# Performance work log

Hardware: AMD Instinct MI355X
Metric: run time of the kernel (lower is better)

Reference implementation:

```python
import jax, jax.numpy as jnp
import numpy as np

NEG = -1e9  # stand-in for -inf mask fill (avoids NaN, softmax weight ~0)
EPS = 1e-5  # torch LayerNorm default


def layer_norm(x, g, b):
    mu = jnp.mean(x, axis=-1, keepdims=True)
    var = jnp.mean(jnp.square(x - mu), axis=-1, keepdims=True)
    return (x - mu) * jax.lax.rsqrt(var + EPS) * g + b


def _forward(x, context, batch_lengths, max_len,
             Wq1, Wk1, Wv1, Wq2, Wk2, Wv2,
             ln1_g, ln1_b, ln2_g, ln2_b, ln3_g, ln3_b,
             fc1_w, fc1_b, fc2_w, fc2_b):
    B, L, E = x.shape
    H, _, dk = Wq1.shape
    pos = jnp.arange(L)
    valid = pos[None, :] < batch_lengths[:, None]                  # [B,L]
    out_mask = valid[:, :, None].astype(x.dtype)                   # [B,L,1] (outputMask)
    key_bias = jnp.where(valid, 0.0, NEG)[:, None, None, :]        # [B,1,1,L] (attnMask on keys)
    causal_bias = jnp.where(pos[:, None] >= pos[None, :], 0.0, NEG)  # [L,L] decoding mask
    scale = 1.0 / jnp.sqrt(jnp.asarray(dk, x.dtype))

    def mha(qk_src, v_src, Wq, Wk, Wv, causal):
        # Q,K from qk_src, V from v_src (faithful to Head.forward)
        m = out_mask[:, None]                                      # [B,1,L,1]
        Q = jnp.einsum('ble,hed->bhld', qk_src, Wq) * m
        K = jnp.einsum('ble,hed->bhld', qk_src, Wk) * m
        V = jnp.einsum('ble,hed->bhld', v_src, Wv) * m
        e = jnp.einsum('bhid,bhjd->bhij', Q, K) + key_bias
        if causal:
            e = e + causal_bias
        s = jax.nn.softmax(e * scale, axis=-1)
        o = jnp.einsum('bhij,bhjd->bhid', s, V)
        return o.transpose(0, 2, 1, 3).reshape(B, L, E)            # concat heads

    z = mha(x, x, Wq1, Wk1, Wv1, causal=True) * out_mask
    x1 = layer_norm(x + z, ln1_g, ln1_b)
    # cross block: Q,K from context, V from x1 (as in source)
    z = mha(context, x1, Wq2, Wk2, Wv2, causal=False) * out_mask
    x2 = layer_norm(x1 + z, ln2_g, ln2_b)
    h = jax.nn.relu(x2 @ fc1_w + fc1_b) * out_mask
    z = (h @ fc2_w + fc2_b) * out_mask
    return layer_norm(x2 + z, ln3_g, ln3_b)


def setup_inputs() -> dict:
    B, L, E, H = 8, 1024, 1024, 16
    dk = E // H
    key = jax.random.key(0)
    ks = jax.random.split(key, 16)
    w = lambda k, s: jax.random.normal(k, s, jnp.float32) * 0.02
    return {
        'x': jax.random.normal(ks[0], (B, L, E), jnp.float32),
        'context': jax.random.normal(ks[1], (B, L, E), jnp.float32),
        'batch_lengths': jax.random.randint(ks[2], (B,), 1, L + 1),
        'max_len': L,
        'Wq1': w(ks[3], (H, E, dk)), 'Wk1': w(ks[4], (H, E, dk)), 'Wv1': w(ks[5], (H, E, dk)),
        'Wq2': w(ks[6], (H, E, dk)), 'Wk2': w(ks[7], (H, E, dk)), 'Wv2': w(ks[8], (H, E, dk)),
        'ln1_g': jnp.ones((E,), jnp.float32), 'ln1_b': jnp.zeros((E,), jnp.float32),
        'ln2_g': jnp.ones((E,), jnp.float32), 'ln2_b': jnp.zeros((E,), jnp.float32),
        'ln3_g': jnp.ones((E,), jnp.float32), 'ln3_b': jnp.zeros((E,), jnp.float32),
        'fc1_w': w(ks[9], (E, E)), 'fc1_b': jnp.zeros((E,), jnp.float32),
        'fc2_w': w(ks[10], (E, E)), 'fc2_b': jnp.zeros((E,), jnp.float32),
    }


def reference(x, context, batch_lengths, max_len,
              Wq1, Wk1, Wv1, Wq2, Wk2, Wv2,
              ln1_g, ln1_b, ln2_g, ln2_b, ln3_g, ln3_b,
              fc1_w, fc1_b, fc2_w, fc2_b):
    return _forward(x, context, batch_lengths, max_len,
                    Wq1, Wk1, Wv1, Wq2, Wk2, Wv2,
                    ln1_g, ln1_b, ln2_g, ln2_b, ln3_g, ln3_b,
                    fc1_w, fc1_b, fc2_w, fc2_b)
```

## Files before the change

kernel.cpp:

```cpp
#include <hip/hip_runtime.h>


typedef unsigned short u16;
typedef unsigned int u32;
typedef __attribute__((ext_vector_type(8))) short bf16x8;
typedef __attribute__((ext_vector_type(4))) float f32x4;

#define Bv 8
#define Lv 1024
#define Ev 1024
#define Hv 16
#define DKv 64
#define Mv (Bv * Lv)

#if defined(__has_builtin)
# if __has_builtin(__builtin_amdgcn_global_load_lds)
#  define HAS_GLL 1
# endif
#endif
#ifndef HAS_GLL
# define HAS_GLL 0
#endif

#if HAS_GLL
__device__ __forceinline__ void gll16(const u16* g, u16* l) {
    __builtin_amdgcn_global_load_lds(
        (const __attribute__((address_space(1))) void*)(unsigned long long)(g),
        (__attribute__((address_space(3))) void*)(unsigned)(unsigned long long)(l),
        16, 0, 0);
}
#endif

#define FENCE() asm volatile("" ::: "memory")

__device__ __forceinline__ u16 f2bf(float f) {
    u32 u = __float_as_uint(f);
    u += 0x7fffu + ((u >> 16) & 1u);
    return (u16)(u >> 16);
}
__device__ __forceinline__ u32 pack2(float a, float b) {
    u32 ua = __float_as_uint(a); ua += 0x7fffu + ((ua >> 16) & 1u);
    u32 ub = __float_as_uint(b); ub += 0x7fffu + ((ub >> 16) & 1u);
    return (ua >> 16) | (ub & 0xffff0000u);
}
__device__ __forceinline__ float bf_lo(u32 u) { return __uint_as_float(u << 16); }
__device__ __forceinline__ float bf_hi(u32 u) { return __uint_as_float(u & 0xffff0000u); }

__global__ __launch_bounds__(256) void prep_k(
    const float* __restrict__ x, const float* __restrict__ ctx,
    const float* __restrict__ wq1, const float* __restrict__ wk1, const float* __restrict__ wv1,
    const float* __restrict__ wq2, const float* __restrict__ wk2, const float* __restrict__ wv2,
    const float* __restrict__ f1, const float* __restrict__ f2,
    u16* __restrict__ xb, u16* __restrict__ cb, u16* __restrict__ WT) {
    const int id = blockIdx.x, t = threadIdx.x;
    if (id < 16384) {
        const float* s = (id < 8192) ? x : ctx;
        u16* d = (id < 8192) ? xb : cb;
        const int i4 = ((id & 8191) * 256 + t) * 4;
        float4 v = *(const float4*)(s + i4);
        uint2 o = {pack2(v.x, v.y), pack2(v.z, v.w)};
        *(uint2*)(d + i4) = o;
        return;
    }
    __shared__ float tl[32][33];
    const int tx = t & 31, ty = t >> 5;
    if (id < 16384 + 6144) {
        const int wi = (id - 16384) >> 10;
        const int tile = (id - 16384) & 1023;
        const float* s = (wi == 0) ? wq1 : (wi == 1) ? wk1 : (wi == 2) ? wv1
                       : (wi == 3) ? wq2 : (wi == 4) ? wk2 : wv2;
        u16* d = WT + (size_t)wi * Ev * Ev;
        const int h = tile >> 6, rem = tile & 63;
        const int d0 = (rem & 1) * 32, e0 = (rem >> 1) * 32;
#pragma unroll
        for (int i = 0; i < 4; i++)
            tl[ty + i * 8][tx] = s[(size_t)h * Ev * DKv + (size_t)(e0 + ty + i * 8) * DKv + d0 + tx];
        __syncthreads();
#pragma unroll
        for (int i = 0; i < 4; i++)
            d[(size_t)(h * DKv + d0 + ty + i * 8) * Ev + e0 + tx] = f2bf(tl[tx][ty + i * 8]);
    } else {
        const int wi = (id - 16384 - 6144) >> 10;
        const int tile = (id - 16384 - 6144) & 1023;
        const float* s = wi ? f2 : f1;
        u16* d = WT + (size_t)(6 + wi) * Ev * Ev;
        const int n0 = (tile & 31) * 32, k0 = (tile >> 5) * 32;
#pragma unroll
        for (int i = 0; i < 4; i++)
            tl[ty + i * 8][tx] = s[(size_t)(k0 + ty + i * 8) * Ev + n0 + tx];
        __syncthreads();
#pragma unroll
        for (int i = 0; i < 4; i++)
            d[(size_t)(n0 + ty + i * 8) * Ev + k0 + tx] = f2bf(tl[tx][ty + i * 8]);
    }
}

template <int BIAS, int RELU, int TRANSW>
__global__ __launch_bounds__(256, 4) void mgemm(const u16* __restrict__ A,
                                                const u16* __restrict__ Wt,
                                                const float* __restrict__ bias,
                                                u16* __restrict__ O0, u16* __restrict__ O1,
                                                u16* __restrict__ O2,
                                                const int* __restrict__ lens,
                                                const u16* __restrict__ A2) {
    __shared__ u16 Alds[2][8 * 512];
    __shared__ u16 Blds[2][8 * 512];
    const int tid = threadIdx.x;
    const int w = tid >> 6, l = tid & 63;
    const int lc = l & 15, lq = l >> 4;
    const int row0 = blockIdx.y * 128, col0 = blockIdx.x * 128;
    const int which = col0 >> 10, colL = col0 & 1023;
    u16* C = (which == 0) ? O0 : (which == 1 ? O1 : O2);
    const bool tr = (TRANSW == which);
    const u16* Aop = (A2 != nullptr && which == 2) ? A2 : A;

    int len = lens[row0 >> 10];
    len = min(max(len, 0), Lv);
    if ((row0 & (Lv - 1)) >= len) {
        const int rr = tid >> 1, cc = (tid & 1) * 64;
        u16* p = tr ? C + (size_t)(colL + rr) * Mv + row0 + cc
                    : C + (size_t)(row0 + rr) * Ev + colL + cc;
        uint4 z4 = {0u, 0u, 0u, 0u};
#pragma unroll
        for (int i = 0; i < 8; i++) *(uint4*)(p + i * 8) = z4;
        return;
    }

    const int wm4 = (w >> 1) * 4, wn4 = (w & 1) * 4;
    f32x4 acc[4][4];
#pragma unroll
    for (int i = 0; i < 4; i++)
#pragma unroll
        for (int j = 0; j < 4; j++) acc[i][j] = (f32x4){0.f, 0.f, 0.f, 0.f};

    const u16* Ag[2]; const u16* Bg[2];
    int lof[2];
#pragma unroll
    for (int i = 0; i < 2; i++) {
        const int s = 2 * w + i;
        Ag[i] = Aop + (size_t)(row0 + s * 16 + lc) * Ev + lq * 8;
        Bg[i] = Wt  + (size_t)(col0 + s * 16 + lc) * Ev + lq * 8;
        lof[i] = s * 512;
    }

#if HAS_GLL
#pragma unroll
    for (int i = 0; i < 2; i++) { gll16(Ag[i], &Alds[0][lof[i]]); gll16(Bg[i], &Blds[0][lof[i]]); }
#pragma unroll
    for (int i = 0; i < 2; i++) { gll16(Ag[i] + 32, &Alds[1][lof[i]]); gll16(Bg[i] + 32, &Blds[1][lof[i]]); }

    for (int t = 0; t < 32; ++t) {
        const int p = t & 1;
        if (t < 31) asm volatile("s_waitcnt vmcnt(4)" ::: "memory");
        else        asm volatile("s_waitcnt vmcnt(0)" ::: "memory");
        __builtin_amdgcn_s_barrier();
        FENCE();
        bf16x8 af[4], bfr[4];
#pragma unroll
        for (int mt = 0; mt < 4; mt++)
            af[mt] = *(const bf16x8*)(&Alds[p][(wm4 + mt) * 512 + l * 8]);
#pragma unroll
        for (int nt = 0; nt < 4; nt++)
            bfr[nt] = *(const bf16x8*)(&Blds[p][(wn4 + nt) * 512 + l * 8]);
#pragma unroll
        for (int mt = 0; mt < 4; mt++)
#pragma unroll
            for (int nt = 0; nt < 4; nt++)
                acc[mt][nt] = __builtin_amdgcn_mfma_f32_16x16x32_bf16(
                    af[mt], bfr[nt], acc[mt][nt], 0, 0, 0);
        FENCE();
        __builtin_amdgcn_s_barrier();
        FENCE();
        if (t < 30) {
            const int ko = (t + 2) * 32;
#pragma unroll
            for (int i = 0; i < 2; i++) {
                gll16(Ag[i] + ko, &Alds[p][lof[i]]);
                gll16(Bg[i] + ko, &Blds[p][lof[i]]);
            }
        }
    }
#else
    for (int t = 0; t < 32; ++t) {
        const int ko = t * 32;
#pragma unroll
        for (int i = 0; i < 2; i++) {
            *(uint4*)(&Alds[0][lof[i] + l * 8]) = *(const uint4*)(Ag[i] + ko);
            *(uint4*)(&Blds[0][lof[i] + l * 8]) = *(const uint4*)(Bg[i] + ko);
        }
        __syncthreads();
        bf16x8 af[4], bfr[4];
#pragma unroll
        for (int mt = 0; mt < 4; mt++)
            af[mt] = *(const bf16x8*)(&Alds[0][(wm4 + mt) * 512 + l * 8]);
#pragma unroll
        for (int nt = 0; nt < 4; nt++)
            bfr[nt] = *(const bf16x8*)(&Blds[0][(wn4 + nt) * 512 + l * 8]);
#pragma unroll
        for (int mt = 0; mt < 4; mt++)
#pragma unroll
            for (int nt = 0; nt < 4; nt++)
                acc[mt][nt] = __builtin_amdgcn_mfma_f32_16x16x32_bf16(
                    af[mt], bfr[nt], acc[mt][nt], 0, 0, 0);
        __syncthreads();
    }
#endif

    float bv[4];
#pragma unroll
    for (int nt = 0; nt < 4; nt++)
        bv[nt] = BIAS ? bias[colL + wn4 * 16 + nt * 16 + lc] : 0.f;

#pragma unroll
    for (int mt = 0; mt < 4; mt++) {
        const int rowb = row0 + wm4 * 16 + mt * 16 + lq * 4;
#pragma unroll
        for (int nt = 0; nt < 4; nt++) {
            const int col = colL + wn4 * 16 + nt * 16 + lc;
            float v[4];
#pragma unroll
            for (int r = 0; r < 4; r++) {
                float xv = acc[mt][nt][r] + bv[nt];
                if (RELU) xv = fmaxf(xv, 0.f);
                v[r] = (((rowb + r) & (Lv - 1)) >= len) ? 0.f : xv;
            }
            if (tr) {
                uint2 o = {pack2(v[0], v[1]), pack2(v[2], v[3])};
                *(uint2*)(C + (size_t)col * Mv + rowb) = o;
            } else {
#pragma unroll
                for (int r = 0; r < 4; r++)
                    C[(size_t)(rowb + r) * Ev + col] = f2bf(v[r]);
            }
        }
    }
}

template <int CAUSAL>
__global__ __launch_bounds__(256) void mattn(u16* __restrict__ QZ,
                                             const u16* __restrict__ K,
                                             const u16* __restrict__ VT,
                                             const int* __restrict__ lens) {
    __shared__ u16 Kt[2][16 * 512];
    __shared__ u16 Vt[2][16 * 512];
    __shared__ u16 Pt[4 * 4 * 512];
    const int b = blockIdx.z, h = blockIdx.y, qb = blockIdx.x;
    const int q0 = qb * 128;
    const int tid = threadIdx.x;
    const int w = tid >> 6, l = tid & 63;
    const int lc = l & 15, lq = l >> 4;
    int len = lens[b];
    len = min(max(len, 0), Lv);

    if (q0 >= len) {
        const int zr = tid >> 1, zc = (tid & 1) * 32;
        uint4 z4 = {0u, 0u, 0u, 0u};
        uint4* p = (uint4*)(QZ + (size_t)(b * Lv + q0 + zr) * Ev + h * DKv + zc);
        p[0] = z4; p[1] = z4; p[2] = z4; p[3] = z4;
        return;
    }

    bf16x8 qf[2][2];
#pragma unroll
    for (int mt = 0; mt < 2; mt++)
#pragma unroll
        for (int k2 = 0; k2 < 2; k2++)
            qf[mt][k2] = *(const bf16x8*)(QZ + (size_t)(b * Lv + q0 + w * 32 + mt * 16 + lc) * Ev +
                                          h * DKv + k2 * 32 + lq * 8);

    f32x4 of[2][4];
#pragma unroll
    for (int mt = 0; mt < 2; mt++)
#pragma unroll
        for (int nd = 0; nd < 4; nd++) of[mt][nd] = (f32x4){0.f, 0.f, 0.f, 0.f};
    float mrow[2][4], lrow[2][4];
#pragma unroll
    for (int mt = 0; mt < 2; mt++)
#pragma unroll
        for (int r = 0; r < 4; r++) { mrow[mt][r] = -1e30f; lrow[mt][r] = 0.f; }

    const u16* Kg[4]; const u16* Vg[4];
    int kof[4], vof[4];
#pragma unroll
    for (int i = 0; i < 4; i++) {
        const int k16 = 2 * w + (i >> 1), d32 = i & 1;
        Kg[i] = K + (size_t)(b * Lv + k16 * 16 + lc) * Ev + h * DKv + d32 * 32 + lq * 8;
        kof[i] = (k16 * 2 + d32) * 512;
        Vg[i] = VT + (size_t)(h * DKv + w * 16 + lc) * Mv + b * Lv + i * 32 + lq * 8;
        vof[i] = (w * 4 + i) * 512;
    }
    u16* Pw = Pt + w * 2048;

    const int jend = CAUSAL ? min(len, q0 + 128) : len;
    const int ntiles = (jend + 127) >> 7;

#if HAS_GLL
#pragma unroll
    for (int i = 0; i < 4; i++) {
        gll16(Kg[i], &Kt[0][kof[i]]);
        gll16(Vg[i], &Vt[0][vof[i]]);
    }
#endif
#if !HAS_GLL
#pragma unroll
    for (int i = 0; i < 4; i++) {
        *(uint4*)(&Kt[0][kof[i] + l * 8]) = *(const uint4*)Kg[i];
        *(uint4*)(&Vt[0][vof[i] + l * 8]) = *(const uint4*)Vg[i];
    }
    __syncthreads();
#endif

    for (int kt = 0; kt < ntiles; kt++) {
        const int p = kt & 1;
        const int koff = kt * 128;
#if HAS_GLL
        if (kt + 1 < ntiles) {
            const int knext = koff + 128;
#pragma unroll
            for (int i = 0; i < 4; i++) {
                gll16(Kg[i] + (size_t)knext * Ev, &Kt[p ^ 1][kof[i]]);
                gll16(Vg[i] + knext, &Vt[p ^ 1][vof[i]]);
            }
            asm volatile("s_waitcnt vmcnt(8)" ::: "memory");
        } else {
            asm volatile("s_waitcnt vmcnt(0)" ::: "memory");
        }
        __builtin_amdgcn_s_barrier();
        FENCE();
#else
        if (kt > 0) {
            const int kprev = koff;
#pragma unroll
            for (int i = 0; i < 4; i++) {
                *(uint4*)(&Kt[p][kof[i] + l * 8]) = *(const uint4*)(Kg[i] + (size_t)kprev * Ev);
                *(uint4*)(&Vt[p][vof[i] + l * 8]) = *(const uint4*)(Vg[i] + kprev);
            }
            __syncthreads();
        }
#endif
        const u16* Kb = &Kt[p][0];
        const u16* Vb = &Vt[p][0];

        f32x4 sf[2][8];
#pragma unroll
        for (int nt = 0; nt < 8; nt++) {
            bf16x8 kf0 = *(const bf16x8*)(Kb + (nt * 2 + 0) * 512 + l * 8);
            bf16x8 kf1 = *(const bf16x8*)(Kb + (nt * 2 + 1) * 512 + l * 8);
#pragma unroll
            for (int mt = 0; mt < 2; mt++) {
                f32x4 s = (f32x4){0.f, 0.f, 0.f, 0.f};
                s = __builtin_amdgcn_mfma_f32_16x16x32_bf16(qf[mt][0], kf0, s, 0, 0, 0);
                s = __builtin_amdgcn_mfma_f32_16x16x32_bf16(qf[mt][1], kf1, s, 0, 0, 0);
                sf[mt][nt] = s;
            }
        }

        float alpha[2][4];
#pragma unroll
        for (int mt = 0; mt < 2; mt++) {
            float tmax[4] = {-1e30f, -1e30f, -1e30f, -1e30f};
#pragma unroll
            for (int nt = 0; nt < 8; nt++) {
                const int jj = koff + nt * 16 + lc;
                const bool jv = jj < len;
#pragma unroll
                for (int r = 0; r < 4; r++) {
                    const int iq = q0 + w * 32 + mt * 16 + lq * 4 + r;
                    const bool valid = jv && (!CAUSAL || jj <= iq);
                    float e = valid ? sf[mt][nt][r] * 0.125f : -1e30f;
                    sf[mt][nt][r] = e;
                    tmax[r] = fmaxf(tmax[r], e);
                }
            }
#pragma unroll
            for (int r = 0; r < 4; r++) {
#pragma unroll
                for (int d = 1; d < 16; d <<= 1)
                    tmax[r] = fmaxf(tmax[r], __shfl_xor(tmax[r], d, 64));
            }
            float psum[4];
#pragma unroll
            for (int r = 0; r < 4; r++) {
                const float mn = fmaxf(mrow[mt][r], tmax[r]);
                alpha[mt][r] = __expf(mrow[mt][r] - mn);
                mrow[mt][r] = mn;
                psum[r] = 0.f;
            }
#pragma unroll
            for (int nt = 0; nt < 8; nt++)
#pragma unroll
                for (int r = 0; r < 4; r++) {
                    float p2 = __expf(sf[mt][nt][r] - mrow[mt][r]);
                    sf[mt][nt][r] = p2;
                    psum[r] += p2;
                }
#pragma unroll
            for (int r = 0; r < 4; r++) {
#pragma unroll
                for (int d = 1; d < 16; d <<= 1) psum[r] += __shfl_xor(psum[r], d, 64);
                lrow[mt][r] = lrow[mt][r] * alpha[mt][r] + psum[r];
            }
#pragma unroll
            for (int nd = 0; nd < 4; nd++)
#pragma unroll
                for (int r = 0; r < 4; r++) of[mt][nd][r] *= alpha[mt][r];
        }

#pragma unroll
        for (int mt = 0; mt < 2; mt++) {
#pragma unroll
            for (int nt = 0; nt < 8; nt++)
#pragma unroll
                for (int r = 0; r < 4; r++)
                    Pw[(nt >> 1) * 512 +
                       ((2 * (nt & 1) + (lc >> 3)) * 16 + lq * 4 + r) * 8 + (lc & 7)] =
                        f2bf(sf[mt][nt][r]);
#pragma unroll
            for (int km = 0; km < 4; km++) {
                bf16x8 pa = *(const bf16x8*)(Pw + km * 512 + l * 8);
#pragma unroll
                for (int nd = 0; nd < 4; nd++) {
                    bf16x8 vb = *(const bf16x8*)(Vb + (nd * 4 + km) * 512 + l * 8);
                    of[mt][nd] = __builtin_amdgcn_mfma_f32_16x16x32_bf16(pa, vb, of[mt][nd], 0, 0, 0);
                }
            }
        }
#if HAS_GLL
        FENCE();
        __builtin_amdgcn_s_barrier();
        FENCE();
#else
        __syncthreads();
#endif
    }

#pragma unroll
    for (int mt = 0; mt < 2; mt++) {
        float inv[4];
#pragma unroll
        for (int r = 0; r < 4; r++) {
            const int iq = q0 + w * 32 + mt * 16 + lq * 4 + r;
            inv[r] = (iq < len && lrow[mt][r] > 0.f) ? (1.f / lrow[mt][r]) : 0.f;
        }
#pragma unroll
        for (int nd = 0; nd < 4; nd++)
#pragma unroll
            for (int r = 0; r < 4; r++)
                QZ[(size_t)(b * Lv + q0 + w * 32 + mt * 16 + lq * 4 + r) * Ev +
                   h * DKv + nd * 16 + lc] = f2bf(of[mt][nd][r] * inv[r]);
    }
}

template <int BASEBF, int OUTF32>
__global__ __launch_bounds__(256) void ln_k(const void* __restrict__ base,
                                            const u16* __restrict__ z,
                                            const float* __restrict__ g,
                                            const float* __restrict__ bta,
                                            void* __restrict__ out) {
    __shared__ float w1[4], w2[4];
    const int row = blockIdx.x, t = threadIdx.x;
    const int w = t >> 6, l = t & 63;
    const int c0 = t * 4;
    float v[4];
    if (BASEBF) {
        uint2 bu = *(const uint2*)((const u16*)base + (size_t)row * Ev + c0);
        v[0] = bf_lo(bu.x); v[1] = bf_hi(bu.x); v[2] = bf_lo(bu.y); v[3] = bf_hi(bu.y);
    } else {
        float4 f = *(const float4*)((const float*)base + (size_t)row * Ev + c0);
        v[0] = f.x; v[1] = f.y; v[2] = f.z; v[3] = f.w;
    }
    uint2 zu = *(const uint2*)(z + (size_t)row * Ev + c0);
    v[0] += bf_lo(zu.x); v[1] += bf_hi(zu.x); v[2] += bf_lo(zu.y); v[3] += bf_hi(zu.y);
    float s1 = v[0] + v[1] + v[2] + v[3];
    float s2 = v[0] * v[0] + v[1] * v[1] + v[2] * v[2] + v[3] * v[3];
#pragma unroll
    for (int d = 1; d < 64; d <<= 1) {
        s1 += __shfl_xor(s1, d, 64);
        s2 += __shfl_xor(s2, d, 64);
    }
    if (l == 0) { w1[w] = s1; w2[w] = s2; }
    __syncthreads();
    s1 = w1[0] + w1[1] + w1[2] + w1[3];
    s2 = w2[0] + w2[1] + w2[2] + w2[3];
    const float mu = s1 * (1.f / Ev);
    const float var = s2 * (1.f / Ev) - mu * mu;
    const float rinv = rsqrtf(fmaxf(var, 0.f) + 1e-5f);
    float4 gv = *(const float4*)(g + c0);
    float4 bv = *(const float4*)(bta + c0);
    float y[4];
    y[0] = (v[0] - mu) * rinv * gv.x + bv.x;
    y[1] = (v[1] - mu) * rinv * gv.y + bv.y;
    y[2] = (v[2] - mu) * rinv * gv.z + bv.z;
    y[3] = (v[3] - mu) * rinv * gv.w + bv.w;
    if (OUTF32) {
        float4 ow = {y[0], y[1], y[2], y[3]};
        *(float4*)((float*)out + (size_t)row * Ev + c0) = ow;
    } else {
        uint2 ow = {pack2(y[0], y[1]), pack2(y[2], y[3])};
        *(uint2*)((u16*)out + (size_t)row * Ev + c0) = ow;
    }
}

extern "C" void kernel_launch(void* const* d_in, const int* in_sizes, int n_in,
                              void* d_out, int out_size, void* d_ws, size_t ws_size,
                              hipStream_t stream) {
    const float* x    = (const float*)d_in[0];
    const float* ctx  = (const float*)d_in[1];
    const int*   lens = (const int*)d_in[2];
    const float* Wq1 = (const float*)d_in[4];
    const float* Wk1 = (const float*)d_in[5];
    const float* Wv1 = (const float*)d_in[6];
    const float* Wq2 = (const float*)d_in[7];
    const float* Wk2 = (const float*)d_in[8];
    const float* Wv2 = (const float*)d_in[9];
    const float* g1 = (const float*)d_in[10], *b1 = (const float*)d_in[11];
    const float* g2 = (const float*)d_in[12], *b2 = (const float*)d_in[13];
    const float* g3 = (const float*)d_in[14], *b3 = (const float*)d_in[15];
    const float* fc1w = (const float*)d_in[16], *fc1b = (const float*)d_in[17];
    const float* fc2w = (const float*)d_in[18], *fc2b = (const float*)d_in[19];

    const size_t WSZ = (size_t)Ev * Ev;
    const size_t MM  = (size_t)Mv * Ev;
    u16* WT = (u16*)d_ws;
    u16* Wtq1 = WT + 0 * WSZ;
    u16* Wtq2 = WT + 3 * WSZ;
    u16* Wtf1 = WT + 6 * WSZ, *Wtf2 = WT + 7 * WSZ;
    u16* B1 = WT + 8 * WSZ;
    u16* B2 = B1 + MM;
    u16* B3 = B2 + MM;
    u16* B4 = B3 + MM;
    u16* xb = (u16*)d_out;
    u16* cb = xb + MM;

    dim3 gP(24576), gW(24, 64), gG1(8, 64), gA(8, Hv, Bv), gL(Mv);

    prep_k<<<gP, 256, 0, stream>>>(x, ctx, Wq1, Wk1, Wv1, Wq2, Wk2, Wv2, fc1w, fc2w,
                                   xb, cb, WT);

    mgemm<0, 0, 2><<<gW, 256, 0, stream>>>(xb, Wtq1, nullptr, B1, B2, B3, lens, nullptr);
    mattn<1><<<gA, 256, 0, stream>>>(B1, B2, B3, lens);
    ln_k<0, 0><<<gL, 256, 0, stream>>>(x, B1, g1, b1, B2);

    mgemm<0, 0, 2><<<gW, 256, 0, stream>>>(cb, Wtq2, nullptr, B1, B3, B4, lens, B2);
    mattn<0><<<gA, 256, 0, stream>>>(B1, B3, B4, lens);
    ln_k<1, 0><<<gL, 256, 0, stream>>>(B2, B1, g2, b2, B3);

    mgemm<1, 1, -1><<<gG1, 256, 0, stream>>>(B3, Wtf1, fc1b, B1, nullptr, nullptr, lens, nullptr);
    mgemm<1, 0, -1><<<gG1, 256, 0, stream>>>(B1, Wtf2, fc2b, B2, nullptr, nullptr, lens, nullptr);
    ln_k<1, 1><<<gL, 256, 0, stream>>>(B3, B2, g3, b3, d_out);
}
```

Before: 513.2 us.

## Shrink attention key tile to 64, skip rescale, exp2 softmax, reverse causal order

The attention kernel now processes keys in 64-wide tiles instead of 128, halving shared-memory buffers and register arrays, and declares a min-blocks hint of 4 to raise occupancy. Softmax uses exp2 with log2e folded into the scale, skips masking on fully valid tiles, and skips the running-max rescale when no row max grew. Causal blocks are launched in reverse order so the longest query blocks start first. The trade-off is more loop iterations, more barriers per key, and an extra wave-wide vote per tile.

```diff
diff --git a/kernel.cpp b/kernel.cpp
--- a/kernel.cpp
+++ b/kernel.cpp
@@ -236,15 +236,17 @@
     }
 }
 
+#define SCL 0.18033688f
 template <int CAUSAL>
-__global__ __launch_bounds__(256) void mattn(u16* __restrict__ QZ,
-                                             const u16* __restrict__ K,
-                                             const u16* __restrict__ VT,
-                                             const int* __restrict__ lens) {
-    __shared__ u16 Kt[2][16 * 512];
-    __shared__ u16 Vt[2][16 * 512];
-    __shared__ u16 Pt[4 * 4 * 512];
-    const int b = blockIdx.z, h = blockIdx.y, qb = blockIdx.x;
+__global__ __launch_bounds__(256, 4) void mattn(u16* __restrict__ QZ,
+                                                const u16* __restrict__ K,
+                                                const u16* __restrict__ VT,
+                                                const int* __restrict__ lens) {
+    __shared__ u16 Kt[2][8 * 512];
+    __shared__ u16 Vt[2][8 * 512];
+    __shared__ u16 Pt[4 * 2 * 512];
+    const int b = blockIdx.z, h = blockIdx.y;
+    const int qb = CAUSAL ? ((int)gridDim.x - 1 - (int)blockIdx.x) : (int)blockIdx.x;
     const int q0 = qb * 128;
     const int tid = threadIdx.x;
     const int w = tid >> 6, l = tid & 63;
@@ -279,31 +281,29 @@
 #pragma unroll
         for (int r = 0; r < 4; r++) { mrow[mt][r] = -1e30f; lrow[mt][r] = 0.f; }
 
-    const u16* Kg[4]; const u16* Vg[4];
-    int kof[4], vof[4];
-#pragma unroll
-    for (int i = 0; i < 4; i++) {
-        const int k16 = 2 * w + (i >> 1), d32 = i & 1;
-        Kg[i] = K + (size_t)(b * Lv + k16 * 16 + lc) * Ev + h * DKv + d32 * 32 + lq * 8;
-        kof[i] = (k16 * 2 + d32) * 512;
+    const u16* Kg[2]; const u16* Vg[2];
+    int kof[2], vof[2];
+#pragma unroll
+    for (int i = 0; i < 2; i++) {
+        Kg[i] = K + (size_t)(b * Lv + w * 16 + lc) * Ev + h * DKv + i * 32 + lq * 8;
+        kof[i] = (w * 2 + i) * 512;
         Vg[i] = VT + (size_t)(h * DKv + w * 16 + lc) * Mv + b * Lv + i * 32 + lq * 8;
-        vof[i] = (w * 4 + i) * 512;
-    }
-    u16* Pw = Pt + w * 2048;
+        vof[i] = (w * 2 + i) * 512;
+    }
+    u16* Pw = Pt + w * 1024;
 
     const int jend = CAUSAL ? min(len, q0 + 128) : len;
-    const int ntiles = (jend + 127) >> 7;
+    const int ntiles = (jend + 63) >> 6;
 
 #if HAS_GLL
 #pragma unroll
-    for (int i = 0; i < 4; i++) {
+    for (int i = 0; i < 2; i++) {
         gll16(Kg[i], &Kt[0][kof[i]]);
         gll16(Vg[i], &Vt[0][vof[i]]);
     }
-#endif
-#if !HAS_GLL
-#pragma unroll
-    for (int i = 0; i < 4; i++) {
+#else
+#pragma unroll
+    for (int i = 0; i < 2; i++) {
         *(uint4*)(&Kt[0][kof[i] + l * 8]) = *(const uint4*)Kg[i];
         *(uint4*)(&Vt[0][vof[i] + l * 8]) = *(const uint4*)Vg[i];
     }
@@ -312,16 +312,16 @@
 
     for (int kt = 0; kt < ntiles; kt++) {
         const int p = kt & 1;
-        const int koff = kt * 128;
+        const int koff = kt * 64;
 #if HAS_GLL
         if (kt + 1 < ntiles) {
-            const int knext = koff + 128;
-#pragma unroll
-            for (int i = 0; i < 4; i++) {
+            const int knext = koff + 64;
+#pragma unroll
+            for (int i = 0; i < 2; i++) {
                 gll16(Kg[i] + (size_t)knext * Ev, &Kt[p ^ 1][kof[i]]);
                 gll16(Vg[i] + knext, &Vt[p ^ 1][vof[i]]);
             }
-            asm volatile("s_waitcnt vmcnt(8)" ::: "memory");
+            asm volatile("s_waitcnt vmcnt(4)" ::: "memory");
         } else {
             asm volatile("s_waitcnt vmcnt(0)" ::: "memory");
         }
@@ -329,11 +329,10 @@
         FENCE();
 #else
         if (kt > 0) {
-            const int kprev = koff;
-#pragma unroll
-            for (int i = 0; i < 4; i++) {
-                *(uint4*)(&Kt[p][kof[i] + l * 8]) = *(const uint4*)(Kg[i] + (size_t)kprev * Ev);
-                *(uint4*)(&Vt[p][vof[i] + l * 8]) = *(const uint4*)(Vg[i] + kprev);
+#pragma unroll
+            for (int i = 0; i < 2; i++) {
+                *(uint4*)(&Kt[p][kof[i] + l * 8]) = *(const uint4*)(Kg[i] + (size_t)koff * Ev);
+                *(uint4*)(&Vt[p][vof[i] + l * 8]) = *(const uint4*)(Vg[i] + koff);
             }
             __syncthreads();
         }
@@ -341,9 +340,9 @@
         const u16* Kb = &Kt[p][0];
         const u16* Vb = &Vt[p][0];
 
-        f32x4 sf[2][8];
-#pragma unroll
-        for (int nt = 0; nt < 8; nt++) {
+        f32x4 sf[2][4];
+#pragma unroll
+        for (int nt = 0; nt < 4; nt++) {
             bf16x8 kf0 = *(const bf16x8*)(Kb + (nt * 2 + 0) * 512 + l * 8);
             bf16x8 kf1 = *(const bf16x8*)(Kb + (nt * 2 + 1) * 512 + l * 8);
 #pragma unroll
@@ -355,21 +354,33 @@
             }
         }
 
-        float alpha[2][4];
 #pragma unroll
         for (int mt = 0; mt < 2; mt++) {
+            const int iqbase = q0 + w * 32 + mt * 16;
             float tmax[4] = {-1e30f, -1e30f, -1e30f, -1e30f};
-#pragma unroll
-            for (int nt = 0; nt < 8; nt++) {
-                const int jj = koff + nt * 16 + lc;
-                const bool jv = jj < len;
-#pragma unroll
-                for (int r = 0; r < 4; r++) {
-                    const int iq = q0 + w * 32 + mt * 16 + lq * 4 + r;
-                    const bool valid = jv && (!CAUSAL || jj <= iq);
-                    float e = valid ? sf[mt][nt][r] * 0.125f : -1e30f;
-                    sf[mt][nt][r] = e;
-                    tmax[r] = fmaxf(tmax[r], e);
+            const bool full = (koff + 64 <= len) && (!CAUSAL || (koff + 63 <= iqbase));
+            if (full) {
+#pragma unroll
+                for (int nt = 0; nt < 4; nt++)
+#pragma unroll
+                    for (int r = 0; r < 4; r++) {
+                        float e = sf[mt][nt][r] * SCL;
+                        sf[mt][nt][r] = e;
+                        tmax[r] = fmaxf(tmax[r], e);
+                    }
+            } else {
+#pragma unroll
+                for (int nt = 0; nt < 4; nt++) {
+                    const int jj = koff + nt * 16 + lc;
+                    const bool jv = jj < len;
+#pragma unroll
+                    for (int r = 0; r < 4; r++) {
+                        const int iq = iqbase + lq * 4 + r;
+                        const bool valid = jv && (!CAUSAL || jj <= iq);
+                        float e = valid ? sf[mt][nt][r] * SCL : -1e30f;
+                        sf[mt][nt][r] = e;
+                        tmax[r] = fmaxf(tmax[r], e);
+                    }
                 }
             }
 #pragma unroll
@@ -378,19 +389,32 @@
                 for (int d = 1; d < 16; d <<= 1)
                     tmax[r] = fmaxf(tmax[r], __shfl_xor(tmax[r], d, 64));
             }
+            bool grow = false;
+#pragma unroll
+            for (int r = 0; r < 4; r++) grow = grow || (tmax[r] > mrow[mt][r]);
             float psum[4];
-#pragma unroll
-            for (int r = 0; r < 4; r++) {
-                const float mn = fmaxf(mrow[mt][r], tmax[r]);
-                alpha[mt][r] = __expf(mrow[mt][r] - mn);
-                mrow[mt][r] = mn;
-                psum[r] = 0.f;
-            }
-#pragma unroll
-            for (int nt = 0; nt < 8; nt++)
+            if (__any(grow)) {
+                float alpha[4];
 #pragma unroll
                 for (int r = 0; r < 4; r++) {
-                    float p2 = __expf(sf[mt][nt][r] - mrow[mt][r]);
+                    const float mn = fmaxf(mrow[mt][r], tmax[r]);
+                    alpha[r] = exp2f(mrow[mt][r] - mn);
+                    mrow[mt][r] = mn;
+                }
+#pragma unroll
+                for (int r = 0; r < 4; r++) lrow[mt][r] *= alpha[r];
+#pragma unroll
+                for (int nd = 0; nd < 4; nd++)
+#pragma unroll
+                    for (int r = 0; r < 4; r++) of[mt][nd][r] *= alpha[r];
+            }
+#pragma unroll
+            for (int r = 0; r < 4; r++) psum[r] = 0.f;
+#pragma unroll
+            for (int nt = 0; nt < 4; nt++)
+#pragma unroll
+                for (int r = 0; r < 4; r++) {
+                    float p2 = exp2f(sf[mt][nt][r] - mrow[mt][r]);
                     sf[mt][nt][r] = p2;
                     psum[r] += p2;
                 }
@@ -398,29 +422,25 @@
             for (int r = 0; r < 4; r++) {
 #pragma unroll
                 for (int d = 1; d < 16; d <<= 1) psum[r] += __shfl_xor(psum[r], d, 64);
-                lrow[mt][r] = lrow[mt][r] * alpha[mt][r] + psum[r];
-            }
-#pragma unroll
-            for (int nd = 0; nd < 4; nd++)
-#pragma unroll
-                for (int r = 0; r < 4; r++) of[mt][nd][r] *= alpha[mt][r];
+                lrow[mt][r] += psum[r];
+            }
         }
 
 #pragma unroll
         for (int mt = 0; mt < 2; mt++) {
 #pragma unroll
-            for (int nt = 0; nt < 8; nt++)
+            for (int nt = 0; nt < 4; nt++)
 #pragma unroll
                 for (int r = 0; r < 4; r++)
                     Pw[(nt >> 1) * 512 +
                        ((2 * (nt & 1) + (lc >> 3)) * 16 + lq * 4 + r) * 8 + (lc & 7)] =
                         f2bf(sf[mt][nt][r]);
 #pragma unroll
-            for (int km = 0; km < 4; km++) {
+            for (int km = 0; km < 2; km++) {
                 bf16x8 pa = *(const bf16x8*)(Pw + km * 512 + l * 8);
 #pragma unroll
                 for (int nd = 0; nd < 4; nd++) {
-                    bf16x8 vb = *(const bf16x8*)(Vb + (nd * 4 + km) * 512 + l * 8);
+                    bf16x8 vb = *(const bf16x8*)(Vb + (nd * 2 + km) * 512 + l * 8);
                     of[mt][nd] = __builtin_amdgcn_mfma_f32_16x16x32_bf16(pa, vb, of[mt][nd], 0, 0, 0);
                 }
             }
```

Result: slower. 586.1 us (+14.2%).

## Restructure attention to read K/V directly, skip masking and rescale when unneeded

Applied to the files above, without the earlier changes.

The attention kernel stops staging K and V through double-buffered LDS with barriers. Each wave now loads its MFMA fragments straight from global memory and processes one 16-row m-tile at a time. It also switches to an exp2 formulation with a prescaled log2e constant, uses a mask-free fast path for fully valid tiles, and skips the rescale of the running output when no row max grows. The row-sum shuffle reduction is deferred to the end, and causal blocks are launched in reverse order so the long rows start first. The host splits the cross-attention projection into a separate QK GEMM and a V GEMM with a different mgemm mode, which risks behaving differently from the earlier fused call, and the direct global loads give up the LDS reuse of K and V across waves.

```diff
diff --git a/kernel.cpp b/kernel.cpp
--- a/kernel.cpp
+++ b/kernel.cpp
@@ -236,15 +236,15 @@
     }
 }
 
+#define SCL 0.18033688f
 template <int CAUSAL>
 __global__ __launch_bounds__(256) void mattn(u16* __restrict__ QZ,
                                              const u16* __restrict__ K,
                                              const u16* __restrict__ VT,
                                              const int* __restrict__ lens) {
-    __shared__ u16 Kt[2][16 * 512];
-    __shared__ u16 Vt[2][16 * 512];
-    __shared__ u16 Pt[4 * 4 * 512];
-    const int b = blockIdx.z, h = blockIdx.y, qb = blockIdx.x;
+    __shared__ u16 Pt[4][2048];
+    const int b = blockIdx.z, h = blockIdx.y;
+    const int qb = CAUSAL ? ((int)gridDim.x - 1 - (int)blockIdx.x) : (int)blockIdx.x;
     const int q0 = qb * 128;
     const int tid = threadIdx.x;
     const int w = tid >> 6, l = tid & 63;
@@ -273,103 +273,60 @@
     for (int mt = 0; mt < 2; mt++)
 #pragma unroll
         for (int nd = 0; nd < 4; nd++) of[mt][nd] = (f32x4){0.f, 0.f, 0.f, 0.f};
-    float mrow[2][4], lrow[2][4];
+    float mrow[2][4], lrp[2][4];
 #pragma unroll
     for (int mt = 0; mt < 2; mt++)
 #pragma unroll
-        for (int r = 0; r < 4; r++) { mrow[mt][r] = -1e30f; lrow[mt][r] = 0.f; }
-
-    const u16* Kg[4]; const u16* Vg[4];
-    int kof[4], vof[4];
-#pragma unroll
-    for (int i = 0; i < 4; i++) {
-        const int k16 = 2 * w + (i >> 1), d32 = i & 1;
-        Kg[i] = K + (size_t)(b * Lv + k16 * 16 + lc) * Ev + h * DKv + d32 * 32 + lq * 8;
-        kof[i] = (k16 * 2 + d32) * 512;
-        Vg[i] = VT + (size_t)(h * DKv + w * 16 + lc) * Mv + b * Lv + i * 32 + lq * 8;
-        vof[i] = (w * 4 + i) * 512;
-    }
-    u16* Pw = Pt + w * 2048;
+        for (int r = 0; r < 4; r++) { mrow[mt][r] = -1e30f; lrp[mt][r] = 0.f; }
+
+    const u16* Kbase = K  + (size_t)(b * Lv + lc) * Ev + h * DKv + lq * 8;
+    const u16* Vbase = VT + (size_t)(h * DKv + lc) * Mv + (size_t)b * Lv + lq * 8;
+    u16* Pw = Pt[w];
 
     const int jend = CAUSAL ? min(len, q0 + 128) : len;
     const int ntiles = (jend + 127) >> 7;
 
-#if HAS_GLL
-#pragma unroll
-    for (int i = 0; i < 4; i++) {
-        gll16(Kg[i], &Kt[0][kof[i]]);
-        gll16(Vg[i], &Vt[0][vof[i]]);
-    }
-#endif
-#if !HAS_GLL
-#pragma unroll
-    for (int i = 0; i < 4; i++) {
-        *(uint4*)(&Kt[0][kof[i] + l * 8]) = *(const uint4*)Kg[i];
-        *(uint4*)(&Vt[0][vof[i] + l * 8]) = *(const uint4*)Vg[i];
-    }
-    __syncthreads();
-#endif
-
     for (int kt = 0; kt < ntiles; kt++) {
-        const int p = kt & 1;
         const int koff = kt * 128;
-#if HAS_GLL
-        if (kt + 1 < ntiles) {
-            const int knext = koff + 128;
-#pragma unroll
-            for (int i = 0; i < 4; i++) {
-                gll16(Kg[i] + (size_t)knext * Ev, &Kt[p ^ 1][kof[i]]);
-                gll16(Vg[i] + knext, &Vt[p ^ 1][vof[i]]);
-            }
-            asm volatile("s_waitcnt vmcnt(8)" ::: "memory");
-        } else {
-            asm volatile("s_waitcnt vmcnt(0)" ::: "memory");
-        }
-        __builtin_amdgcn_s_barrier();
-        FENCE();
-#else
-        if (kt > 0) {
-            const int kprev = koff;
-#pragma unroll
-            for (int i = 0; i < 4; i++) {
-                *(uint4*)(&Kt[p][kof[i] + l * 8]) = *(const uint4*)(Kg[i] + (size_t)kprev * Ev);
-                *(uint4*)(&Vt[p][vof[i] + l * 8]) = *(const uint4*)(Vg[i] + kprev);
-            }
-            __syncthreads();
-        }
-#endif
-        const u16* Kb = &Kt[p][0];
-        const u16* Vb = &Vt[p][0];
-
-        f32x4 sf[2][8];
-#pragma unroll
-        for (int nt = 0; nt < 8; nt++) {
-            bf16x8 kf0 = *(const bf16x8*)(Kb + (nt * 2 + 0) * 512 + l * 8);
-            bf16x8 kf1 = *(const bf16x8*)(Kb + (nt * 2 + 1) * 512 + l * 8);
-#pragma unroll
-            for (int mt = 0; mt < 2; mt++) {
+#pragma unroll
+        for (int mt = 0; mt < 2; mt++) {
+            const int iqbase = q0 + w * 32 + mt * 16;
+            f32x4 sf[8];
+#pragma unroll
+            for (int nt = 0; nt < 8; nt++) {
+                const u16* kp = Kbase + (size_t)(koff + nt * 16) * Ev;
+                bf16x8 kf0 = *(const bf16x8*)(kp);
+                bf16x8 kf1 = *(const bf16x8*)(kp + 32);
                 f32x4 s = (f32x4){0.f, 0.f, 0.f, 0.f};
                 s = __builtin_amdgcn_mfma_f32_16x16x32_bf16(qf[mt][0], kf0, s, 0, 0, 0);
                 s = __builtin_amdgcn_mfma_f32_16x16x32_bf16(qf[mt][1], kf1, s, 0, 0, 0);
-                sf[mt][nt] = s;
-            }
-        }
-
-        float alpha[2][4];
-#pragma unroll
-        for (int mt = 0; mt < 2; mt++) {
+                sf[nt] = s;
+            }
+
             float tmax[4] = {-1e30f, -1e30f, -1e30f, -1e30f};
-#pragma unroll
-            for (int nt = 0; nt < 8; nt++) {
-                const int jj = koff + nt * 16 + lc;
-                const bool jv = jj < len;
-#pragma unroll
-                for (int r = 0; r < 4; r++) {
-                    const int iq = q0 + w * 32 + mt * 16 + lq * 4 + r;
-                    const bool valid = jv && (!CAUSAL || jj <= iq);
-                    float e = valid ? sf[mt][nt][r] * 0.125f : -1e30f;
-                    sf[mt][nt][r] = e;
-                    tmax[r] = fmaxf(tmax[r], e);
+            const bool full = (koff + 128 <= len) && (!CAUSAL || (koff + 127 <= iqbase));
+            if (full) {
+#pragma unroll
+                for (int nt = 0; nt < 8; nt++)
+#pragma unroll
+                    for (int r = 0; r < 4; r++) {
+                        float e = sf[nt][r] * SCL;
+                        sf[nt][r] = e;
+                        tmax[r] = fmaxf(tmax[r], e);
+                    }
+            } else {
+#pragma unroll
+                for (int nt = 0; nt < 8; nt++) {
+                    const int jj = koff + nt * 16 + lc;
+                    const bool jv = jj < len;
+#pragma unroll
+                    for (int r = 0; r < 4; r++) {
+                        const int iq = iqbase + lq * 4 + r;
+                        const bool valid = jv && (!CAUSAL || jj <= iq);
+                        float e = valid ? sf[nt][r] * SCL : -1e30f;
+                        sf[nt][r] = e;
+                        tmax[r] = fmaxf(tmax[r], e);
+                    }
                 }
             }
 #pragma unroll
@@ -378,60 +335,51 @@
                 for (int d = 1; d < 16; d <<= 1)
                     tmax[r] = fmaxf(tmax[r], __shfl_xor(tmax[r], d, 64));
             }
-            float psum[4];
-#pragma unroll
-            for (int r = 0; r < 4; r++) {
-                const float mn = fmaxf(mrow[mt][r], tmax[r]);
-                alpha[mt][r] = __expf(mrow[mt][r] - mn);
-                mrow[mt][r] = mn;
-                psum[r] = 0.f;
+            bool grow = false;
+#pragma unroll
+            for (int r = 0; r < 4; r++) grow = grow || (tmax[r] > mrow[mt][r]);
+            if (__any(grow)) {
+                float alpha[4];
+#pragma unroll
+                for (int r = 0; r < 4; r++) {
+                    const float mn = fmaxf(mrow[mt][r], tmax[r]);
+                    alpha[r] = exp2f(mrow[mt][r] - mn);
+                    mrow[mt][r] = mn;
+                }
+#pragma unroll
+                for (int r = 0; r < 4; r++) lrp[mt][r] *= alpha[r];
+#pragma unroll
+                for (int nd = 0; nd < 4; nd++)
+#pragma unroll
+                    for (int r = 0; r < 4; r++) of[mt][nd][r] *= alpha[r];
             }
 #pragma unroll
             for (int nt = 0; nt < 8; nt++)
 #pragma unroll
                 for (int r = 0; r < 4; r++) {
-                    float p2 = __expf(sf[mt][nt][r] - mrow[mt][r]);
-                    sf[mt][nt][r] = p2;
-                    psum[r] += p2;
+                    float p2 = exp2f(sf[nt][r] - mrow[mt][r]);
+                    sf[nt][r] = p2;
+                    lrp[mt][r] += p2;
                 }
-#pragma unroll
-            for (int r = 0; r < 4; r++) {
-#pragma unroll
-                for (int d = 1; d < 16; d <<= 1) psum[r] += __shfl_xor(psum[r], d, 64);
-                lrow[mt][r] = lrow[mt][r] * alpha[mt][r] + psum[r];
-            }
-#pragma unroll
-            for (int nd = 0; nd < 4; nd++)
-#pragma unroll
-                for (int r = 0; r < 4; r++) of[mt][nd][r] *= alpha[mt][r];
-        }
-
-#pragma unroll
-        for (int mt = 0; mt < 2; mt++) {
+
 #pragma unroll
             for (int nt = 0; nt < 8; nt++)
 #pragma unroll
                 for (int r = 0; r < 4; r++)
                     Pw[(nt >> 1) * 512 +
                        ((2 * (nt & 1) + (lc >> 3)) * 16 + lq * 4 + r) * 8 + (lc & 7)] =
-                        f2bf(sf[mt][nt][r]);
+                        f2bf(sf[nt][r]);
 #pragma unroll
             for (int km = 0; km < 4; km++) {
                 bf16x8 pa = *(const bf16x8*)(Pw + km * 512 + l * 8);
 #pragma unroll
                 for (int nd = 0; nd < 4; nd++) {
-                    bf16x8 vb = *(const bf16x8*)(Vb + (nd * 4 + km) * 512 + l * 8);
+                    bf16x8 vb = *(const bf16x8*)(Vbase + (size_t)(nd * 16) * Mv +
+                                                 koff + km * 32);
                     of[mt][nd] = __builtin_amdgcn_mfma_f32_16x16x32_bf16(pa, vb, of[mt][nd], 0, 0, 0);
                 }
             }
         }
-#if HAS_GLL
-        FENCE();
-        __builtin_amdgcn_s_barrier();
-        FENCE();
-#else
-        __syncthreads();
-#endif
     }
 
 #pragma unroll
@@ -439,8 +387,11 @@
         float inv[4];
 #pragma unroll
         for (int r = 0; r < 4; r++) {
+            float ls = lrp[mt][r];
+#pragma unroll
+            for (int d = 1; d < 16; d <<= 1) ls += __shfl_xor(ls, d, 64);
             const int iq = q0 + w * 32 + mt * 16 + lq * 4 + r;
-            inv[r] = (iq < len && lrow[mt][r] > 0.f) ? (1.f / lrow[mt][r]) : 0.f;
+            inv[r] = (iq < len && ls > 0.f) ? (1.f / ls) : 0.f;
         }
 #pragma unroll
         for (int nd = 0; nd < 4; nd++)
@@ -523,7 +474,7 @@
     const size_t MM  = (size_t)Mv * Ev;
     u16* WT = (u16*)d_ws;
     u16* Wtq1 = WT + 0 * WSZ;
-    u16* Wtq2 = WT + 3 * WSZ;
+    u16* Wtq2 = WT + 3 * WSZ, *Wtv2 = WT + 5 * WSZ;
     u16* Wtf1 = WT + 6 * WSZ, *Wtf2 = WT + 7 * WSZ;
     u16* B1 = WT + 8 * WSZ;
     u16* B2 = B1 + MM;
@@ -532,16 +483,17 @@
     u16* xb = (u16*)d_out;
     u16* cb = xb + MM;
 
-    dim3 gP(24576), gW(24, 64), gG1(8, 64), gA(8, Hv, Bv), gL(Mv);
+    dim3 gP(24576), gQKV(24, 64), gQK(16, 64), gG1(8, 64), gA(8, Hv, Bv), gL(Mv);
 
     prep_k<<<gP, 256, 0, stream>>>(x, ctx, Wq1, Wk1, Wv1, Wq2, Wk2, Wv2, fc1w, fc2w,
                                    xb, cb, WT);
 
-    mgemm<0, 0, 2><<<gW, 256, 0, stream>>>(xb, Wtq1, nullptr, B1, B2, B3, lens, nullptr);
+    mgemm<0, 0, 2><<<gQKV, 256, 0, stream>>>(xb, Wtq1, nullptr, B1, B2, B3, lens, nullptr);
     mattn<1><<<gA, 256, 0, stream>>>(B1, B2, B3, lens);
     ln_k<0, 0><<<gL, 256, 0, stream>>>(x, B1, g1, b1, B2);
 
-    mgemm<0, 0, 2><<<gW, 256, 0, stream>>>(cb, Wtq2, nullptr, B1, B3, B4, lens, B2);
+    mgemm<0, 0, -1><<<gQK, 256, 0, stream>>>(cb, Wtq2, nullptr, B1, B3, nullptr, lens, nullptr);
+    mgemm<0, 0, 0><<<gG1, 256, 0, stream>>>(B2, Wtv2, nullptr, B4, nullptr, nullptr, lens, nullptr);
     mattn<0><<<gA, 256, 0, stream>>>(B1, B3, B4, lens);
     ln_k<1, 0><<<gL, 256, 0, stream>>>(B2, B1, g2, b2, B3);
 
```

Measured after the change: 661.6 us. 28.9% more time.

## Streamline attention softmax: exp2 scaling, mask fast path, deferred row-sum, reversed causal order

Applied to the files above, without the earlier changes.

The attention kernel now folds log2(e) into the score scale so it can use exp2f, and skips per-element masking on tiles that are fully valid. It rescales the output only when some lane's running max actually grew, and keeps per-lane partial row sums, doing the cross-lane reduction once at the end instead of every tile. Causal blocks are launched in reverse so the longest query blocks start first, for better load balance. These cut VALU and shuffle work in the softmax inner loop, at the cost of more branching and a small change in numerical rounding.

```diff
diff --git a/kernel.cpp b/kernel.cpp
--- a/kernel.cpp
+++ b/kernel.cpp
@@ -236,6 +236,7 @@
     }
 }
 
+#define SCL 0.18033688f
 template <int CAUSAL>
 __global__ __launch_bounds__(256) void mattn(u16* __restrict__ QZ,
                                              const u16* __restrict__ K,
@@ -244,7 +245,8 @@
     __shared__ u16 Kt[2][16 * 512];
     __shared__ u16 Vt[2][16 * 512];
     __shared__ u16 Pt[4 * 4 * 512];
-    const int b = blockIdx.z, h = blockIdx.y, qb = blockIdx.x;
+    const int b = blockIdx.z, h = blockIdx.y;
+    const int qb = CAUSAL ? ((int)gridDim.x - 1 - (int)blockIdx.x) : (int)blockIdx.x;
     const int q0 = qb * 128;
     const int tid = threadIdx.x;
     const int w = tid >> 6, l = tid & 63;
@@ -273,11 +275,11 @@
     for (int mt = 0; mt < 2; mt++)
 #pragma unroll
         for (int nd = 0; nd < 4; nd++) of[mt][nd] = (f32x4){0.f, 0.f, 0.f, 0.f};
-    float mrow[2][4], lrow[2][4];
+    float mrow[2][4], lrp[2][4];
 #pragma unroll
     for (int mt = 0; mt < 2; mt++)
 #pragma unroll
-        for (int r = 0; r < 4; r++) { mrow[mt][r] = -1e30f; lrow[mt][r] = 0.f; }
+        for (int r = 0; r < 4; r++) { mrow[mt][r] = -1e30f; lrp[mt][r] = 0.f; }
 
     const u16* Kg[4]; const u16* Vg[4];
     int kof[4], vof[4];
@@ -300,8 +302,7 @@
         gll16(Kg[i], &Kt[0][kof[i]]);
         gll16(Vg[i], &Vt[0][vof[i]]);
     }
-#endif
-#if !HAS_GLL
+#else
 #pragma unroll
     for (int i = 0; i < 4; i++) {
         *(uint4*)(&Kt[0][kof[i] + l * 8]) = *(const uint4*)Kg[i];
@@ -355,21 +356,33 @@
             }
         }
 
-        float alpha[2][4];
 #pragma unroll
         for (int mt = 0; mt < 2; mt++) {
+            const int iqbase = q0 + w * 32 + mt * 16;
             float tmax[4] = {-1e30f, -1e30f, -1e30f, -1e30f};
-#pragma unroll
-            for (int nt = 0; nt < 8; nt++) {
-                const int jj = koff + nt * 16 + lc;
-                const bool jv = jj < len;
-#pragma unroll
-                for (int r = 0; r < 4; r++) {
-                    const int iq = q0 + w * 32 + mt * 16 + lq * 4 + r;
-                    const bool valid = jv && (!CAUSAL || jj <= iq);
-                    float e = valid ? sf[mt][nt][r] * 0.125f : -1e30f;
-                    sf[mt][nt][r] = e;
-                    tmax[r] = fmaxf(tmax[r], e);
+            const bool full = (koff + 128 <= len) && (!CAUSAL || (koff + 127 <= iqbase));
+            if (full) {
+#pragma unroll
+                for (int nt = 0; nt < 8; nt++)
+#pragma unroll
+                    for (int r = 0; r < 4; r++) {
+                        float e = sf[mt][nt][r] * SCL;
+                        sf[mt][nt][r] = e;
+                        tmax[r] = fmaxf(tmax[r], e);
+                    }
+            } else {
+#pragma unroll
+                for (int nt = 0; nt < 8; nt++) {
+                    const int jj = koff + nt * 16 + lc;
+                    const bool jv = jj < len;
+#pragma unroll
+                    for (int r = 0; r < 4; r++) {
+                        const int iq = iqbase + lq * 4 + r;
+                        const bool valid = jv && (!CAUSAL || jj <= iq);
+                        float e = valid ? sf[mt][nt][r] * SCL : -1e30f;
+                        sf[mt][nt][r] = e;
+                        tmax[r] = fmaxf(tmax[r], e);
+                    }
                 }
             }
 #pragma unroll
@@ -378,32 +391,32 @@
                 for (int d = 1; d < 16; d <<= 1)
                     tmax[r] = fmaxf(tmax[r], __shfl_xor(tmax[r], d, 64));
             }
-            float psum[4];
-#pragma unroll
-            for (int r = 0; r < 4; r++) {
-                const float mn = fmaxf(mrow[mt][r], tmax[r]);
-                alpha[mt][r] = __expf(mrow[mt][r] - mn);
-                mrow[mt][r] = mn;
-                psum[r] = 0.f;
+            bool grow = false;
+#pragma unroll
+            for (int r = 0; r < 4; r++) grow = grow || (tmax[r] > mrow[mt][r]);
+            if (__any(grow)) {
+                float alpha[4];
+#pragma unroll
+                for (int r = 0; r < 4; r++) {
+                    const float mn = fmaxf(mrow[mt][r], tmax[r]);
+                    alpha[r] = exp2f(mrow[mt][r] - mn);
+                    mrow[mt][r] = mn;
+                }
+#pragma unroll
+                for (int r = 0; r < 4; r++) lrp[mt][r] *= alpha[r];
+#pragma unroll
+                for (int nd = 0; nd < 4; nd++)
+#pragma unroll
+                    for (int r = 0; r < 4; r++) of[mt][nd][r] *= alpha[r];
             }
 #pragma unroll
             for (int nt = 0; nt < 8; nt++)
 #pragma unroll
                 for (int r = 0; r < 4; r++) {
-                    float p2 = __expf(sf[mt][nt][r] - mrow[mt][r]);
+                    float p2 = exp2f(sf[mt][nt][r] - mrow[mt][r]);
                     sf[mt][nt][r] = p2;
-                    psum[r] += p2;
+                    lrp[mt][r] += p2;
                 }
-#pragma unroll
-            for (int r = 0; r < 4; r++) {
-#pragma unroll
-                for (int d = 1; d < 16; d <<= 1) psum[r] += __shfl_xor(psum[r], d, 64);
-                lrow[mt][r] = lrow[mt][r] * alpha[mt][r] + psum[r];
-            }
-#pragma unroll
-            for (int nd = 0; nd < 4; nd++)
-#pragma unroll
-                for (int r = 0; r < 4; r++) of[mt][nd][r] *= alpha[mt][r];
         }
 
 #pragma unroll
@@ -439,8 +452,11 @@
         float inv[4];
 #pragma unroll
         for (int r = 0; r < 4; r++) {
+            float ls = lrp[mt][r];
+#pragma unroll
+            for (int d = 1; d < 16; d <<= 1) ls += __shfl_xor(ls, d, 64);
             const int iq = q0 + w * 32 + mt * 16 + lq * 4 + r;
-            inv[r] = (iq < len && lrow[mt][r] > 0.f) ? (1.f / lrow[mt][r]) : 0.f;
+            inv[r] = (iq < len && ls > 0.f) ? (1.f / ls) : 0.f;
         }
 #pragma unroll
         for (int nd = 0; nd < 4; nd++)
```

After: 543.4 us. 5.9% more time.
